# Performance work log

Hardware: AMD Instinct MI355X
Metric: run time of the kernel (lower is better)

Reference implementation:

```python
import jax, jax.numpy as jnp
import numpy as np

B, T, I, H, V = 128, 80, 4096, 256, 6000
DEC_STEPS = 40


def _lstm_cell(x, h, c, Wih, Whh, b):
    # PyTorch gate order: i, f, g, o
    gates = x @ Wih.T + h @ Whh.T + b  # (B, 4H)
    i, f, g, o = jnp.split(gates, 4, axis=-1)
    c_new = jax.nn.sigmoid(f) * c + jax.nn.sigmoid(i) * jnp.tanh(g)
    h_new = jax.nn.sigmoid(o) * jnp.tanh(c_new)
    return h_new, c_new


def _lstm_scan(xs, h0, c0, Wih, Whh, b):
    # xs: (T, B, D)
    def step(carry, x):
        h, c = carry
        h, c = _lstm_cell(x, h, c, Wih, Whh, b)
        return (h, c), h
    (h, c), ys = jax.lax.scan(step, (h0, c0), xs)
    return ys, h, c


def setup_inputs() -> dict:
    key = jax.random.key(0)
    ks = jax.random.split(key, 11)
    s = 1.0 / np.sqrt(H)  # pytorch default LSTM init scale
    return {
        "x": jax.random.normal(ks[0], (B, T, I), jnp.float32),
        "W_ih1": jax.random.uniform(ks[1], (4 * H, I), jnp.float32, -s, s),
        "W_hh1": jax.random.uniform(ks[2], (4 * H, H), jnp.float32, -s, s),
        "b_ih1": jax.random.uniform(ks[3], (4 * H,), jnp.float32, -s, s),
        "b_hh1": jax.random.uniform(ks[4], (4 * H,), jnp.float32, -s, s),
        "W_ih2": jax.random.uniform(ks[5], (4 * H, H), jnp.float32, -s, s),
        "W_hh2": jax.random.uniform(ks[6], (4 * H, H), jnp.float32, -s, s),
        "b_ih2": jax.random.uniform(ks[7], (4 * H,), jnp.float32, -s, s),
        "b_ih2": jax.random.uniform(ks[7], (4 * H,), jnp.float32, -s, s),
        "b_hh2": jax.random.uniform(ks[8], (4 * H,), jnp.float32, -s, s),
        "W_out": jax.random.uniform(ks[9], (V, H), jnp.float32, -s, s),
        "b_out": jax.random.uniform(ks[10], (V,), jnp.float32, -s, s),
    }


def reference(x, W_ih1, W_hh1, b_ih1, b_hh1, W_ih2, W_hh2, b_ih2, b_hh2, W_out, b_out):
    batch = x.shape[0]
    b1 = b_ih1 + b_hh1
    b2 = b_ih2 + b_hh2
    z = jnp.zeros((batch, H), x.dtype)

    # --- Encoding: lstm1 over video features, lstm2 over lstm1 outputs ---
    xs = jnp.transpose(x, (1, 0, 2))  # (T, B, I)
    ys1, h1, c1 = _lstm_scan(xs, z, z, W_ih1, W_hh1, b1)
    _, h2, c2 = _lstm_scan(ys1, z, z, W_ih2, W_hh2, b2)

    # --- One extra lstm1 step with zero padding (as in the source) ---
    dec_pad = jnp.zeros((batch, I), x.dtype)
    h1, c1 = _lstm_cell(dec_pad, h1, c1, W_ih1, W_hh1, b1)
    y2 = jnp.zeros((batch, H), x.dtype)

    def dec_step(carry, _):
        h1, c1, h2, c2, y2 = carry
        h1, c1 = _lstm_cell(dec_pad, h1, c1, W_ih1, W_hh1, b1)
        h2, c2 = _lstm_cell(h1 + y2, h2, c2, W_ih2, W_hh2, b2)
        return (h1, c1, h2, c2, h2), h2

    _, ys = jax.lax.scan(dec_step, (h1, c1, h2, c2, y2), None, length=DEC_STEPS)  # (40, B, H)
    feats = jnp.transpose(ys, (1, 0, 2)).reshape(-1, H)  # (B*40, H)
    return feats @ W_out.T + b_out  # (B*40, V)
```

## Files before the change

### kernel.cpp

```cpp
#include <hip/hip_runtime.h>

#define NB 128
#define NT 80
#define NI 4096
#define NH 256
#define G4 1024
#define NV 6000
#define NVP 6016
#define NDEC 40

typedef unsigned short ushort_t;
typedef __attribute__((ext_vector_type(8))) short bf16x8;
typedef __attribute__((ext_vector_type(4))) float f32x4;

__device__ __forceinline__ unsigned short f2bf(float f) {
  unsigned int x = __float_as_uint(f);
  x += 0x7FFFu + ((x >> 16) & 1u);
  return (unsigned short)(x >> 16);
}
__device__ __forceinline__ ushort4 pack4(float4 v) {
  return make_ushort4(f2bf(v.x), f2bf(v.y), f2bf(v.z), f2bf(v.w));
}
__device__ __forceinline__ float ftanh(float x) {
  float xc = fminf(fmaxf(x, -12.f), 12.f);
  float e = __expf(2.f * xc);
  return (e - 1.f) * __builtin_amdgcn_rcpf(e + 1.f);
}
__device__ __forceinline__ float fsig(float x) {
  return __builtin_amdgcn_rcpf(1.f + __expf(-x));
}


__global__ __launch_bounds__(256) void k_cast_x(const float* __restrict__ x,
                                                ushort_t* __restrict__ xb) {
  const int t = blockIdx.x, b = blockIdx.y;
  const float* src = x + ((size_t)b * NT + t) * NI;
  ushort_t* dst = xb + ((size_t)t * NB + b) * NI;
#pragma unroll
  for (int s = 0; s < 4; ++s) {
    int j = s * 1024 + threadIdx.x * 4;
    float4 v = *(const float4*)(src + j);
    *(ushort4*)(dst + j) = pack4(v);
  }
}

__global__ __launch_bounds__(256) void k_cast_pad(const float* __restrict__ s,
                                                  ushort_t* __restrict__ d,
                                                  int nsrc, int ndst) {
  int i = (blockIdx.x * 256 + threadIdx.x) * 4;
  if (i >= ndst) return;
  ushort4 o;
  if (i < nsrc) {
    float4 v = *(const float4*)(s + i);
    o = pack4(v);
  } else {
    o = make_ushort4(0, 0, 0, 0);
  }
  *(ushort4*)(d + i) = o;
}

__global__ __launch_bounds__(256) void k_addw_bf(const float* __restrict__ a,
                                                 const float* __restrict__ b,
                                                 ushort_t* __restrict__ o) {
  int i = (blockIdx.x * 256 + threadIdx.x) * 4;
  float4 va = *(const float4*)(a + i);
  float4 vb = *(const float4*)(b + i);
  va.x += vb.x; va.y += vb.y; va.z += vb.z; va.w += vb.w;
  *(ushort4*)(o + i) = pack4(va);
}


#define GLDS(gp, lp)                                                     \
  __builtin_amdgcn_global_load_lds(                                      \
      (const __attribute__((address_space(1))) unsigned int*)(gp),       \
      (__attribute__((address_space(3))) unsigned int*)(lp), 16, 0, 0)

__global__ __launch_bounds__(256) void k_gemm(
    const ushort_t* __restrict__ A, const ushort_t* __restrict__ Bm,
    float* __restrict__ C, const float* __restrict__ ba,
    const float* __restrict__ bb, int Nreal, int K, int ldc, int mtiles) {
  __shared__ __align__(16) ushort_t Als[128 * 32];
  __shared__ __align__(16) ushort_t Bls[128 * 32];
  const int bid = blockIdx.x;
  const int mt = bid % mtiles, nt = bid / mtiles;
  const size_t m0 = (size_t)mt * 128, n0 = (size_t)nt * 128;
  const int tid = threadIdx.x, wave = tid >> 6, lane = tid & 63;
  const int wm = (wave & 1) * 64, wn = (wave >> 1) * 64;
  const int srow = wave * 16 + (lane >> 2), skcol = (lane & 3) * 8;
  const int fr = lane & 15, kb = (lane >> 4) * 8;

  f32x4 acc[4][4];
#pragma unroll
  for (int i = 0; i < 4; ++i)
#pragma unroll
    for (int j = 0; j < 4; ++j) acc[i][j] = (f32x4){0.f, 0.f, 0.f, 0.f};

  for (int kk = 0; kk < K; kk += 32) {
    __syncthreads();
#pragma unroll
    for (int p = 0; p < 2; ++p) {
      GLDS(A + (m0 + p * 64 + srow) * K + kk + skcol,
           &Als[(p * 64 + wave * 16) * 32]);
      GLDS(Bm + (n0 + p * 64 + srow) * K + kk + skcol,
           &Bls[(p * 64 + wave * 16) * 32]);
    }
    __syncthreads();
    bf16x8 af[4], bfr[4];
#pragma unroll
    for (int i = 0; i < 4; ++i)
      af[i] = *(const bf16x8*)&Als[(wm + i * 16 + fr) * 32 + kb];
#pragma unroll
    for (int j = 0; j < 4; ++j)
      bfr[j] = *(const bf16x8*)&Bls[(wn + j * 16 + fr) * 32 + kb];
#pragma unroll
    for (int i = 0; i < 4; ++i)
#pragma unroll
      for (int j = 0; j < 4; ++j)
        acc[i][j] = __builtin_amdgcn_mfma_f32_16x16x32_bf16(af[i], bfr[j],
                                                            acc[i][j], 0, 0, 0);
  }
  const int cr4 = (lane >> 4) * 4, ccn = lane & 15;
#pragma unroll
  for (int j = 0; j < 4; ++j) {
    int n = (int)n0 + wn + j * 16 + ccn;
    if (n < Nreal) {
      float bv = (ba ? ba[n] : 0.f) + (bb ? bb[n] : 0.f);
#pragma unroll
      for (int i = 0; i < 4; ++i) {
#pragma unroll
        for (int r = 0; r < 4; ++r) {
          size_t m = m0 + wm + i * 16 + cr4 + r;
          C[m * (size_t)ldc + n] = acc[i][j][r] + bv;
        }
      }
    }
  }
}


#define LOAD_WREGS(Wb)                                                        \
  _Pragma("unroll") for (int g = 0; g < 3; ++g)                               \
  _Pragma("unroll") for (int h = 0; h < 2; ++h)                               \
  _Pragma("unroll") for (int kb = 0; kb < 8; ++kb)                            \
      wr[g * 2 + h][kb] = *(const bf16x8*)((Wb) +                             \
          (size_t)(g * 256 + cbase + h * 16 + cn) * NH + kb * 32 + kgrp * 8);

#define PIN_W()                                                               \
  _Pragma("unroll") for (int g = 0; g < 6; ++g)                               \
  _Pragma("unroll") for (int kb = 0; kb < 8; ++kb)                            \
      asm volatile("" : "+a"(wr[g][kb]));

#define LOAD_WLDS(Wb)                                                         \
  _Pragma("unroll") for (int h = 0; h < 2; ++h)                               \
  _Pragma("unroll") for (int kb = 0; kb < 8; ++kb)                            \
      *(bf16x8*)&WL[wv * 8192 + h * 4096 + kb * 512 + cn * 32 + kgrp * 8] =   \
          *(const bf16x8*)((Wb) +                                             \
          (size_t)(768 + cbase + h * 16 + cn) * NH + kb * 32 + kgrp * 8);

__global__ __launch_bounds__(512, 1) void p_lstm16(
    const float* __restrict__ gIn0, const float* __restrict__ gIn1, int n0,
    int nTot, const ushort_t* __restrict__ W0, const ushort_t* __restrict__ Wsw,
    int swStep, const float* __restrict__ biasA, const float* __restrict__ biasB,
    ushort_t* __restrict__ traj0, ushort_t* __restrict__ traj1, int t1bmaj) {
  __shared__ __align__(16) ushort_t WL[8 * 8192];
  __shared__ __align__(16) ushort_t hTz[2][16 * 264];
  const int tid = threadIdx.x;
  const int bg = blockIdx.x;
  const int wv = tid >> 6, lane = tid & 63;
  const int cn = lane & 15;
  const int kgrp = lane >> 4;
  const int cbase = wv * 32;
  const int rsel = kgrp & 1;

  bf16x8 wr[6][8];
  LOAD_WREGS(W0);
  PIN_W();
  LOAD_WLDS(W0);
  for (int i = tid; i < 2 * 16 * 264; i += 512) ((ushort_t*)hTz)[i] = 0;

  float cs[8];
#pragma unroll
  for (int i = 0; i < 8; ++i) cs[i] = 0.f;
  __syncthreads();

  int cur = 0;
  for (int t = 0; t < nTot; ++t) {
    if (Wsw && t == swStep) {
      LOAD_WREGS(Wsw);
      PIN_W();
      LOAD_WLDS(Wsw);
      __syncthreads();
    }
    const ushort_t* hTc = &hTz[cur][0];
    ushort_t* hTn = &hTz[cur ^ 1][0];
    const float* gseg = (t < n0) ? gIn0 : gIn1;
    const int tt = (t < n0) ? t : t - n0;
#pragma unroll
    for (int h = 0; h < 2; ++h) {
      const int gcol = cbase + h * 16 + cn;
      float in_[4][4];
      if (gseg) {
        const float* base = gseg + (size_t)tt * (NB * G4);
#pragma unroll
        for (int g = 0; g < 4; ++g)
#pragma unroll
          for (int e = 0; e < 4; ++e)
            in_[g][e] = base[(size_t)(bg * 8 + rsel * 4 + e) * G4 + g * 256 + gcol];
      } else {
#pragma unroll
        for (int g = 0; g < 4; ++g) {
          float b = biasA[g * 256 + gcol] + biasB[g * 256 + gcol];
#pragma unroll
          for (int e = 0; e < 4; ++e) in_[g][e] = b;
        }
      }
      f32x4 acc[4];
#pragma unroll
      for (int g = 0; g < 4; ++g) acc[g] = (f32x4){0.f, 0.f, 0.f, 0.f};
#pragma unroll
      for (int kb = 0; kb < 8; ++kb) {
        bf16x8 af = *(const bf16x8*)&hTc[cn * 264 + kb * 32 + kgrp * 8];
        bf16x8 bo = *(const bf16x8*)&WL[wv * 8192 + h * 4096 + kb * 512 +
                                        cn * 32 + kgrp * 8];
        acc[0] = __builtin_amdgcn_mfma_f32_16x16x32_bf16(af, wr[0 + h][kb],
                                                         acc[0], 0, 0, 0);
        acc[1] = __builtin_amdgcn_mfma_f32_16x16x32_bf16(af, wr[2 + h][kb],
                                                         acc[1], 0, 0, 0);
        acc[2] = __builtin_amdgcn_mfma_f32_16x16x32_bf16(af, wr[4 + h][kb],
                                                         acc[2], 0, 0, 0);
        acc[3] = __builtin_amdgcn_mfma_f32_16x16x32_bf16(af, bo, acc[3], 0, 0, 0);
      }
#pragma unroll
      for (int e = 0; e < 4; ++e) {
        float a0 = acc[0][e] + in_[0][e];
        float a1 = acc[1][e] + in_[1][e];
        float a2 = acc[2][e] + in_[2][e];
        float a3 = acc[3][e] + in_[3][e];
        float ig = fsig(a0);
        float fg = fsig(a1);
        float gg = ftanh(a2);
        float og = fsig(a3);
        float cn_ = fg * cs[h * 4 + e] + ig * gg;
        cs[h * 4 + e] = cn_;
        float hn = og * ftanh(cn_);
        unsigned short hb = f2bf(hn);
        if (lane < 32) {
          const int b = (lane >> 4) * 4 + e;
          hTn[b * 264 + gcol] = hb;
          const int bglob = bg * 8 + b;
          if (t < n0) {
            if (traj0)
              traj0[(size_t)t * (NB * NH) + (size_t)bglob * NH + gcol] = hb;
          } else if (traj1) {
            size_t idx =
                t1bmaj ? ((size_t)bglob * NDEC + (t - n0)) * NH + gcol
                       : (size_t)(t - n0) * (NB * NH) + (size_t)bglob * NH + gcol;
            traj1[idx] = hb;
          }
        }
      }
    }
    __syncthreads();
    cur ^= 1;
  }
}


extern "C" void kernel_launch(void* const* d_in, const int* in_sizes, int n_in,
                              void* d_out, int out_size, void* d_ws,
                              size_t ws_size, hipStream_t stream) {
  const float* x = (const float*)d_in[0];
  const float* Wih1 = (const float*)d_in[1];
  const float* Whh1 = (const float*)d_in[2];
  const float* bih1 = (const float*)d_in[3];
  const float* bhh1 = (const float*)d_in[4];
  const float* Wih2 = (const float*)d_in[5];
  const float* Whh2 = (const float*)d_in[6];
  const float* bih2 = (const float*)d_in[7];
  const float* bhh2 = (const float*)d_in[8];
  const float* Wout = (const float*)d_in[9];
  const float* bout = (const float*)d_in[10];
  char* ws = (char*)d_ws;

  ushort_t* x_bf   = (ushort_t*)(ws + 0);
  float*    Gbuf3  = (float*)(ws + 0);
  float*    Gbuf   = (float*)(ws + 83886080);
  ushort_t* Wih1b  = (ushort_t*)(ws + 125829120);
  ushort_t* Wih2b  = (ushort_t*)(ws + 134217728);
  ushort_t* Woutb  = (ushort_t*)(ws + 134742016);
  ushort_t* Whh1b  = (ushort_t*)(ws + 137822208);
  ushort_t* Whh2b  = (ushort_t*)(ws + 138346496);
  ushort_t* ys1    = (ushort_t*)(ws + 138870784);
  ushort_t* H1dec  = (ushort_t*)(ws + 144113664);
  ushort_t* feats  = (ushort_t*)(ws + 146800640);
  ushort_t* Wsumb  = (ushort_t*)(ws + 149422080);

  k_cast_x<<<dim3(NT, NB), 256, 0, stream>>>(x, x_bf);
  k_cast_pad<<<4096, 256, 0, stream>>>(Wih1, Wih1b, G4 * NI, G4 * NI);
  k_cast_pad<<<256, 256, 0, stream>>>(Wih2, Wih2b, G4 * NH, G4 * NH);
  k_cast_pad<<<1504, 256, 0, stream>>>(Wout, Woutb, NV * NH, NVP * NH);
  k_cast_pad<<<256, 256, 0, stream>>>(Whh1, Whh1b, G4 * NH, G4 * NH);
  k_cast_pad<<<256, 256, 0, stream>>>(Whh2, Whh2b, G4 * NH, G4 * NH);
  k_addw_bf<<<256, 256, 0, stream>>>(Wih2, Whh2, Wsumb);

  k_gemm<<<640, 256, 0, stream>>>(x_bf, Wih1b, Gbuf, bih1, bhh1, G4, NI, G4, 80);

  p_lstm16<<<16, 512, 0, stream>>>(Gbuf, nullptr, NT, NT + NDEC + 1, Whh1b,
                                   nullptr, 1 << 30, bih1, bhh1, ys1, H1dec, 0);

  k_gemm<<<640, 256, 0, stream>>>(ys1, Wih2b, Gbuf, bih2, bhh2, G4, NH, G4, 80);
  k_gemm<<<320, 256, 0, stream>>>(H1dec + (size_t)NB * NH, Wih2b, Gbuf3, bih2,
                                  bhh2, G4, NH, G4, 40);

  p_lstm16<<<16, 512, 0, stream>>>(Gbuf, Gbuf3, NT, NT + NDEC, Whh2b, Wsumb,
                                   NT + 1, nullptr, nullptr, nullptr, feats, 1);

  k_gemm<<<40 * 47, 256, 0, stream>>>(feats, Woutb, (float*)d_out, bout, nullptr,
                                      NV, NH, NV, 40);
}
```

Before: 1.464 ms.

## Split LSTM chains into segments and overlap layer1 and layer2 in dual kernels

Splits each recurrent LSTM chain into 40-step segments that save and restore h/c state through workspace buffers. A dual kernel runs the next lstm1 segment on 16 blocks concurrently with the previous lstm2 segment on another 16 blocks, with the input-projection GEMMs interleaved. This shortens the serial critical path of the two recurrences at the cost of extra launches, state save/reload and weight reloads per segment.

```diff
diff --git a/kernel.cpp b/kernel.cpp
--- a/kernel.cpp
+++ b/kernel.cpp
@@ -138,6 +138,14 @@
 }
 
 
+struct ChainArgs {
+  const float* gIn0; const float* gIn1; int n0; int tStart; int tEnd;
+  const ushort_t* W0; const ushort_t* Wsw; int swStep;
+  const float* biasA; const float* biasB;
+  ushort_t* traj0; ushort_t* traj1; int t1bmaj;
+  ushort_t* hSt; float* cSt;
+};
+
 #define LOAD_WREGS(Wb)                                                        \
   _Pragma("unroll") for (int g = 0; g < 3; ++g)                               \
   _Pragma("unroll") for (int h = 0; h < 2; ++h)                               \
@@ -157,15 +165,10 @@
           *(const bf16x8*)((Wb) +                                             \
           (size_t)(768 + cbase + h * 16 + cn) * NH + kb * 32 + kgrp * 8);
 
-__global__ __launch_bounds__(512, 1) void p_lstm16(
-    const float* __restrict__ gIn0, const float* __restrict__ gIn1, int n0,
-    int nTot, const ushort_t* __restrict__ W0, const ushort_t* __restrict__ Wsw,
-    int swStep, const float* __restrict__ biasA, const float* __restrict__ biasB,
-    ushort_t* __restrict__ traj0, ushort_t* __restrict__ traj1, int t1bmaj) {
-  __shared__ __align__(16) ushort_t WL[8 * 8192];
-  __shared__ __align__(16) ushort_t hTz[2][16 * 264];
+__device__ __forceinline__ void run_chain(const ChainArgs a, int bg,
+                                          ushort_t* WL,
+                                          ushort_t (*hTz)[16 * 264]) {
   const int tid = threadIdx.x;
-  const int bg = blockIdx.x;
   const int wv = tid >> 6, lane = tid & 63;
   const int cn = lane & 15;
   const int kgrp = lane >> 4;
@@ -173,28 +176,43 @@
   const int rsel = kgrp & 1;
 
   bf16x8 wr[6][8];
-  LOAD_WREGS(W0);
+  const ushort_t* Winit = (a.Wsw && a.tStart >= a.swStep) ? a.Wsw : a.W0;
+  LOAD_WREGS(Winit);
   PIN_W();
-  LOAD_WLDS(W0);
+  LOAD_WLDS(Winit);
+
   for (int i = tid; i < 2 * 16 * 264; i += 512) ((ushort_t*)hTz)[i] = 0;
-
+  __syncthreads();
   float cs[8];
-#pragma unroll
-  for (int i = 0; i < 8; ++i) cs[i] = 0.f;
+  if (a.tStart == 0) {
+#pragma unroll
+    for (int i = 0; i < 8; ++i) cs[i] = 0.f;
+  } else {
+    for (int i = tid; i < 8 * 256; i += 512) {
+      int b = i >> 8, col = i & 255;
+      hTz[0][b * 264 + col] = a.hSt[(size_t)(bg * 8 + b) * NH + col];
+    }
+#pragma unroll
+    for (int h = 0; h < 2; ++h)
+#pragma unroll
+      for (int e = 0; e < 4; ++e)
+        cs[h * 4 + e] =
+            a.cSt[(size_t)(bg * 8 + rsel * 4 + e) * NH + cbase + h * 16 + cn];
+  }
   __syncthreads();
 
   int cur = 0;
-  for (int t = 0; t < nTot; ++t) {
-    if (Wsw && t == swStep) {
-      LOAD_WREGS(Wsw);
+  for (int t = a.tStart; t < a.tEnd; ++t) {
+    if (a.Wsw && t == a.swStep && t != a.tStart) {
+      LOAD_WREGS(a.Wsw);
       PIN_W();
-      LOAD_WLDS(Wsw);
+      LOAD_WLDS(a.Wsw);
       __syncthreads();
     }
     const ushort_t* hTc = &hTz[cur][0];
     ushort_t* hTn = &hTz[cur ^ 1][0];
-    const float* gseg = (t < n0) ? gIn0 : gIn1;
-    const int tt = (t < n0) ? t : t - n0;
+    const float* gseg = (t < a.n0) ? a.gIn0 : a.gIn1;
+    const int tt = (t < a.n0) ? t : t - a.n0;
 #pragma unroll
     for (int h = 0; h < 2; ++h) {
       const int gcol = cbase + h * 16 + cn;
@@ -209,7 +227,7 @@
       } else {
 #pragma unroll
         for (int g = 0; g < 4; ++g) {
-          float b = biasA[g * 256 + gcol] + biasB[g * 256 + gcol];
+          float b = a.biasA[g * 256 + gcol] + a.biasB[g * 256 + gcol];
 #pragma unroll
           for (int e = 0; e < 4; ++e) in_[g][e] = b;
         }
@@ -248,14 +266,14 @@
           const int b = (lane >> 4) * 4 + e;
           hTn[b * 264 + gcol] = hb;
           const int bglob = bg * 8 + b;
-          if (t < n0) {
-            if (traj0)
-              traj0[(size_t)t * (NB * NH) + (size_t)bglob * NH + gcol] = hb;
-          } else if (traj1) {
-            size_t idx =
-                t1bmaj ? ((size_t)bglob * NDEC + (t - n0)) * NH + gcol
-                       : (size_t)(t - n0) * (NB * NH) + (size_t)bglob * NH + gcol;
-            traj1[idx] = hb;
+          if (t < a.n0) {
+            if (a.traj0)
+              a.traj0[(size_t)t * (NB * NH) + (size_t)bglob * NH + gcol] = hb;
+          } else if (a.traj1) {
+            size_t idx = a.t1bmaj
+                ? ((size_t)bglob * NDEC + (t - a.n0)) * NH + gcol
+                : (size_t)(t - a.n0) * (NB * NH) + (size_t)bglob * NH + gcol;
+            a.traj1[idx] = hb;
           }
         }
       }
@@ -263,6 +281,34 @@
     __syncthreads();
     cur ^= 1;
   }
+
+  for (int i = tid; i < 8 * 256; i += 512) {
+    int b = i >> 8, col = i & 255;
+    a.hSt[(size_t)(bg * 8 + b) * NH + col] = hTz[cur][b * 264 + col];
+  }
+  if (lane < 32) {
+#pragma unroll
+    for (int h = 0; h < 2; ++h)
+#pragma unroll
+      for (int e = 0; e < 4; ++e)
+        a.cSt[(size_t)(bg * 8 + (lane >> 4) * 4 + e) * NH + cbase + h * 16 + cn] =
+            cs[h * 4 + e];
+  }
+}
+
+__global__ __launch_bounds__(512, 1) void p_lstm16(ChainArgs a) {
+  __shared__ __align__(16) ushort_t WL[8 * 8192];
+  __shared__ __align__(16) ushort_t hTz[2][16 * 264];
+  run_chain(a, blockIdx.x, WL, hTz);
+}
+
+__global__ __launch_bounds__(512, 1) void p_dual(ChainArgs a, ChainArgs b) {
+  __shared__ __align__(16) ushort_t WL[8 * 8192];
+  __shared__ __align__(16) ushort_t hTz[2][16 * 264];
+  if (blockIdx.x < 16)
+    run_chain(a, blockIdx.x, WL, hTz);
+  else
+    run_chain(b, blockIdx.x - 16, WL, hTz);
 }
 
 
@@ -283,9 +329,14 @@
   char* ws = (char*)d_ws;
 
   ushort_t* x_bf   = (ushort_t*)(ws + 0);
-  float*    Gbuf3  = (float*)(ws + 0);
+  float*    G2buf  = (float*)(ws + 0);
+  float*    G3buf  = (float*)(ws + 41943040);
   float*    Gbuf   = (float*)(ws + 83886080);
   ushort_t* Wih1b  = (ushort_t*)(ws + 125829120);
+  ushort_t* h1St   = (ushort_t*)(ws + 125829120);
+  float*    c1St   = (float*)(ws + 125894656);
+  ushort_t* h2St   = (ushort_t*)(ws + 126025728);
+  float*    c2St   = (float*)(ws + 126091264);
   ushort_t* Wih2b  = (ushort_t*)(ws + 134217728);
   ushort_t* Woutb  = (ushort_t*)(ws + 134742016);
   ushort_t* Whh1b  = (ushort_t*)(ws + 137822208);
@@ -305,15 +356,33 @@
 
   k_gemm<<<640, 256, 0, stream>>>(x_bf, Wih1b, Gbuf, bih1, bhh1, G4, NI, G4, 80);
 
-  p_lstm16<<<16, 512, 0, stream>>>(Gbuf, nullptr, NT, NT + NDEC + 1, Whh1b,
-                                   nullptr, 1 << 30, bih1, bhh1, ys1, H1dec, 0);
-
-  k_gemm<<<640, 256, 0, stream>>>(ys1, Wih2b, Gbuf, bih2, bhh2, G4, NH, G4, 80);
-  k_gemm<<<320, 256, 0, stream>>>(H1dec + (size_t)NB * NH, Wih2b, Gbuf3, bih2,
+  ChainArgs c1{Gbuf, nullptr, NT, 0, 0, Whh1b, nullptr, 1 << 30,
+               bih1, bhh1, ys1, H1dec, 0, h1St, c1St};
+  ChainArgs c2{G2buf, G3buf, NT, 0, 0, Whh2b, Wsumb, NT + 1,
+               bih2, bhh2, nullptr, feats, 1, h2St, c2St};
+
+  ChainArgs e1a = c1; e1a.tStart = 0; e1a.tEnd = 40;
+  p_lstm16<<<16, 512, 0, stream>>>(e1a);
+
+  k_gemm<<<320, 256, 0, stream>>>(ys1, Wih2b, G2buf, bih2, bhh2, G4, NH, G4, 40);
+
+  ChainArgs e1b = c1; e1b.tStart = 40; e1b.tEnd = 80;
+  ChainArgs e2a = c2; e2a.tStart = 0; e2a.tEnd = 40;
+  p_dual<<<32, 512, 0, stream>>>(e1b, e2a);
+
+  k_gemm<<<320, 256, 0, stream>>>(ys1 + (size_t)40 * NB * NH, Wih2b,
+                                  G2buf + (size_t)40 * NB * G4, bih2, bhh2,
+                                  G4, NH, G4, 40);
+
+  ChainArgs p1 = c1; p1.tStart = 80; p1.tEnd = 121;
+  ChainArgs e2b = c2; e2b.tStart = 40; e2b.tEnd = 80;
+  p_dual<<<32, 512, 0, stream>>>(p1, e2b);
+
+  k_gemm<<<320, 256, 0, stream>>>(H1dec + (size_t)NB * NH, Wih2b, G3buf, bih2,
                                   bhh2, G4, NH, G4, 40);
 
-  p_lstm16<<<16, 512, 0, stream>>>(Gbuf, Gbuf3, NT, NT + NDEC, Whh2b, Wsumb,
-                                   NT + 1, nullptr, nullptr, nullptr, feats, 1);
+  ChainArgs d2 = c2; d2.tStart = 80; d2.tEnd = 120;
+  p_lstm16<<<16, 512, 0, stream>>>(d2);
 
   k_gemm<<<40 * 47, 256, 0, stream>>>(feats, Woutb, (float*)d_out, bout, nullptr,
                                       NV, NH, NV, 40);
```

Result: faster. 1.332 ms (-9.0%).
